# Optimization experiments

Measured on AMD Instinct MI355X. Metric: run time of the kernel, lower is better.

## Reference

```python
import jax, jax.numpy as jnp
from jax import lax
import numpy as np

B, N, C = 8, 50000, 8
SCORE_THR = 0.99
NMS_THR = 0.5
MAX_DET = 100
K_PRE = 1024          # per-class candidate budget (>> expected ~500 survivors of the 0.99 threshold)
NEG = jnp.float32(-1e30)


def setup_inputs() -> dict:
    key = jax.random.key(0)
    k1, k2, k3, k4, k5 = jax.random.split(key, 5)
    # valid (x1,y1,x2,y2) boxes in a 512px frame
    cxy = jax.random.uniform(k1, (B, N, 2), dtype=jnp.float32) * 512.0
    wh = jax.random.uniform(k2, (B, N, 2), dtype=jnp.float32) * 96.0 + 4.0
    boxes = jnp.concatenate([cxy - wh * 0.5, cxy + wh * 0.5], axis=-1)
    classification = jax.random.uniform(k3, (B, N, C), dtype=jnp.float32)
    rotation = jax.random.normal(k4, (B, N, 3), dtype=jnp.float32)
    translation = jax.random.normal(k5, (B, N, 3), dtype=jnp.float32)
    return {"boxes": boxes, "classification": classification,
            "rotation": rotation, "translation": translation}


def _pairwise_iou(b):  # b: [K,4] -> [K,K]
    x1, y1, x2, y2 = b[:, 0], b[:, 1], b[:, 2], b[:, 3]
    area = (x2 - x1) * (y2 - y1)
    iw = jnp.maximum(jnp.minimum(x2[:, None], x2[None, :]) - jnp.maximum(x1[:, None], x1[None, :]), 0.0)
    ih = jnp.maximum(jnp.minimum(y2[:, None], y2[None, :]) - jnp.maximum(y1[:, None], y1[None, :]), 0.0)
    inter = iw * ih
    return inter / (area[:, None] + area[None, :] - inter)


def _nms_one_class(boxes_n, scores_n):
    """boxes_n [N,4], scores_n [N] -> (top_s [K], top_i [K], keep [K] bool)."""
    masked = jnp.where(scores_n > SCORE_THR, scores_n, NEG)
    top_s, top_i = lax.top_k(masked, K_PRE)       # sorted descending, like torchvision NMS ordering
    cand = boxes_n[top_i]                          # [K,4]
    valid = top_s > SCORE_THR
    iou = _pairwise_iou(cand)                      # [K,K]

    def step(keep, i):
        # suppressed if any already-kept higher-score box overlaps > NMS_THR
        suppressed = jnp.any(keep & (iou[:, i] > NMS_THR))
        keep = keep.at[i].set(valid[i] & ~suppressed)
        return keep, None

    keep, _ = lax.scan(step, jnp.zeros(K_PRE, dtype=bool), jnp.arange(K_PRE))
    return top_s, top_i, keep


def _filter(boxes, classification, rotation, translation):
    b, n, c = classification.shape
    per_class = jax.vmap(_nms_one_class, in_axes=(None, 1))      # over classes
    top_s, top_i, keep = jax.vmap(per_class)(boxes, classification)  # [B,C,K] each

    sc = jnp.where(keep, top_s, NEG).reshape(b, c * K_PRE)
    labels = jnp.broadcast_to(jnp.arange(c)[None, :, None], (b, c, K_PRE)).reshape(b, c * K_PRE)
    idx = top_i.reshape(b, c * K_PRE)

    best_s, sel = lax.top_k(sc, MAX_DET)                          # [B,100]
    sel_idx = jnp.take_along_axis(idx, sel, axis=1)
    sel_lab = jnp.take_along_axis(labels, sel, axis=1)
    ok = best_s > SCORE_THR                                       # kept scores are all > threshold

    gather = lambda x: jnp.take_along_axis(x, sel_idx[:, :, None], axis=1)
    out_boxes = jnp.where(ok[:, :, None], gather(boxes), -1.0)
    out_scores = jnp.where(ok, best_s, -1.0)
    out_labels = jnp.where(ok, sel_lab, -1).astype(jnp.int64)
    out_rot = jnp.where(ok[:, :, None], gather(rotation), -1.0)
    out_trans = jnp.where(ok[:, :, None], gather(translation), -1.0)
    return out_boxes, out_scores, out_labels, out_rot, out_trans


@jax.jit
def reference(boxes, classification, rotation, translation):
    return _filter(boxes, classification, rotation, translation)
```

## Files before the change

### kernel.cpp

```cpp
#include <hip/hip_runtime.h>
#include <stdint.h>

#define BB 8
#define NN 50000
#define SCORE_THR 0.99f
#define NMS_THR 0.5f
#define MAX_DET 100
#define K_PRE 1024
#define CAP 2048
#define KEEP_CAP 128
#define CNT_STRIDE 64
#define T_MAX 16
#define NPAIR 136
#define TRI_WORDS 8704

typedef unsigned long long u64;
typedef unsigned int u32;
typedef __attribute__((ext_vector_type(2))) unsigned long long u64x2;


__global__ void k_init(int* __restrict__ cnts) {
    for (int i = threadIdx.x; i < 64 * CNT_STRIDE; i += 256) cnts[i] = 0;
}

__global__ __launch_bounds__(256) void k_filter(const float* __restrict__ cls,
                                                int* __restrict__ cand_cnt,
                                                u64* __restrict__ cand_keys) {
    __shared__ int wcnt[8][4];
    __shared__ int woff[8][4];
    __shared__ int cbase[8];
    int b = blockIdx.y;
    int tid = threadIdx.x;
    int lane = tid & 63, w = tid >> 6;
    int n = blockIdx.x * 256 + tid;
    bool vn = n < NN;
    float s[8];
    if (vn) {
        const float4* p = (const float4*)(cls + ((size_t)b * NN + n) * 8);
        float4 a = p[0], b2 = p[1];
        s[0] = a.x; s[1] = a.y; s[2] = a.z; s[3] = a.w;
        s[4] = b2.x; s[5] = b2.y; s[6] = b2.z; s[7] = b2.w;
    } else {
        #pragma unroll
        for (int c = 0; c < 8; ++c) s[c] = 0.f;
    }
    u64 bal[8];
    #pragma unroll
    for (int c = 0; c < 8; ++c) {
        bool pred = vn && (s[c] > SCORE_THR);
        bal[c] = __ballot(pred);
        if (lane == 0) wcnt[c][w] = (int)__popcll(bal[c]);
    }
    __syncthreads();
    if (tid < 8) {
        int c = tid, acc = 0;
        #pragma unroll
        for (int ww = 0; ww < 4; ++ww) { woff[c][ww] = acc; acc += wcnt[c][ww]; }
        cbase[c] = acc ? atomicAdd(&cand_cnt[(b * 8 + c) * CNT_STRIDE], acc) : 0;
    }
    __syncthreads();
    #pragma unroll
    for (int c = 0; c < 8; ++c) {
        if (vn && (s[c] > SCORE_THR)) {
            int slot = cbase[c] + woff[c][w] + (int)__popcll(bal[c] & ((1ull << lane) - 1ull));
            if (slot < CAP)
                cand_keys[(size_t)(b * 8 + c) * CAP + slot] =
                    ((u64)__float_as_uint(s[c]) << 32) | (u32)(~(u32)n);
        }
    }
}

__global__ __launch_bounds__(64) void k_sort(const float* __restrict__ boxes,
                                             const int* __restrict__ cand_cnt,
                                             const u64* __restrict__ cand_keys,
                                             u64* __restrict__ sk_g,
                                             float4* __restrict__ box4) {
    __shared__ __align__(16) u64 sk_in[CAP];
    int lane = threadIdx.x;
    int q = blockIdx.x;
    int bc = blockIdx.y;
    int b = bc >> 3;
    int cnt = cand_cnt[bc * CNT_STRIDE];
    if (cnt > CAP) cnt = CAP;
    if (q * 64 >= cnt) return;
    int cnt2 = (cnt + 1) & ~1;
    for (int i = lane; i < cnt2; i += 64)
        sk_in[i] = (i < cnt) ? cand_keys[(size_t)bc * CAP + i] : 0ull;
    __syncthreads();
    int i0 = q * 64 + lane;
    u64 k0 = (i0 < cnt) ? sk_in[i0] : 0ull;
    int r0 = 0;
    int nv = cnt2 >> 1;
    const u64x2* skv = (const u64x2*)sk_in;
    #pragma unroll 4
    for (int jv = 0; jv < nv; ++jv) {
        u64x2 kk = skv[jv];
        r0 += (kk.x > k0); r0 += (kk.y > k0);
    }
    if (i0 < cnt && r0 < K_PRE) {
        sk_g[(size_t)bc * K_PRE + r0] = k0;
        u32 n = ~(u32)k0;
        box4[(size_t)bc * K_PRE + r0] =
            *(const float4*)(boxes + ((size_t)b * NN + n) * 4);
    }
}

__global__ __launch_bounds__(256) void k_iou(const int* __restrict__ cand_cnt,
                                             const float4* __restrict__ box4,
                                             u64* __restrict__ rowmask) {
    int bc = blockIdx.y;
    int p = blockIdx.x;
    int cnt = cand_cnt[bc * CNT_STRIDE];
    int n_cand = cnt < K_PRE ? cnt : K_PRE;
    int ntiles = (n_cand + 63) >> 6;
    int ti = 0, acc = 0;
    while (acc + ti + 1 <= p) { acc += ti + 1; ++ti; }
    int tj = p - acc;
    if (ti >= ntiles) return;
    const float4* bx = box4 + (size_t)bc * K_PRE;
    __shared__ float4 srb[64];
    int tid = threadIdx.x;
    int lane = tid & 63, w = tid >> 6;
    if (tid < 64) srb[tid] = bx[ti * 64 + tid];
    __syncthreads();
    int cg = tj * 64 + lane;
    float4 cb = bx[cg];
    float ca = (cb.z - cb.x) * (cb.w - cb.y);
    u64* out = rowmask + (size_t)bc * TRI_WORDS + 64 * (ti * (ti + 1) / 2) + tj;
    #pragma unroll
    for (int r16 = 0; r16 < 16; ++r16) {
        int r = (w << 4) | r16;
        float4 rb = srb[r];
        float ra = (rb.z - rb.x) * (rb.w - rb.y);
        float iw = fminf(rb.z, cb.z) - fmaxf(rb.x, cb.x);
        float ih = fminf(rb.w, cb.w) - fmaxf(rb.y, cb.y);
        iw = fmaxf(iw, 0.f); ih = fmaxf(ih, 0.f);
        float inter = iw * ih;
        float iou = inter / (ra + ca - inter);
        int rg = ti * 64 + r;
        bool pr = (rg < n_cand) && (cg < n_cand) && ((ti != tj) || (lane < r)) &&
                  (iou > NMS_THR);
        u64 m = __ballot(pr);
        if (lane == 0) out[(size_t)r * (ti + 1)] = m;
    }
}

__global__ __launch_bounds__(1024) void k_fuse(const float* __restrict__ boxes,
                                               const float* __restrict__ rot,
                                               const float* __restrict__ trans,
                                               const int* __restrict__ cand_cnt,
                                               const u64* __restrict__ sk_g,
                                               const u64* __restrict__ rowmask,
                                               float* __restrict__ out) {
    __shared__ u64 fk[1024];
    __shared__ int scnt[8];
    int tid = threadIdx.x;
    int lane = tid & 63, w = tid >> 6;
    int b = blockIdx.x;
    fk[tid] = 0ull;
    __syncthreads();
    if (w < 8) {
        int c = w;
        int bc = b * 8 + c;
        int cnt = cand_cnt[bc * CNT_STRIDE];
        int n_cand = cnt < K_PRE ? cnt : K_PRE;
        int ntiles = (n_cand + 63) >> 6;
        const u64* tri = rowmask + (size_t)bc * TRI_WORDS;
        u64 kept_w[T_MAX];
        #pragma unroll
        for (int t = 0; t < T_MAX; ++t) kept_w[t] = 0ull;
        for (int t = 0; t < ntiles; ++t) {
            int g = t * 64 + lane;
            const u64* base = tri + 64 * (t * (t + 1) / 2) + (size_t)lane * (t + 1);
            u64 supbits = 0;
            #pragma unroll
            for (int ww = 0; ww < T_MAX - 1; ++ww)
                if (ww < t) supbits |= base[ww] & kept_w[ww];
            u64 rowm = base[t];
            bool el = (g < n_cand) && (supbits == 0ull);
            u64 alive = __ballot(el);
            u64 kb = 0;
            while (alive) {
                int j = __ffsll(alive) - 1;
                kb |= (1ull << j);
                u64 colj = __ballot(((rowm >> j) & 1ull) != 0);
                alive &= ~(colj | (1ull << j));
            }
            #pragma unroll
            for (int ww = 0; ww < T_MAX; ++ww)
                if (ww == t) kept_w[ww] = kb;
        }
        u64 lmask = (1ull << lane) - 1ull;
        int pre = 0;
        #pragma unroll
        for (int t = 0; t < T_MAX; ++t) {
            if (t < ntiles) {
                u64 kb = kept_w[t];
                if ((kb >> lane) & 1ull) {
                    int rank = pre + (int)__popcll(kb & lmask);
                    if (rank < KEEP_CAP) {
                        int i = t * 64 + lane;
                        u64 key = sk_g[(size_t)bc * K_PRE + i];
                        u32 sb = (u32)(key >> 32);
                        u32 n = (~(u32)key) & 0x1FFFFu;
                        int pos = c * K_PRE + i;
                        fk[c * KEEP_CAP + rank] =
                            ((u64)sb << 30) | ((u64)(8191 - pos) << 17) | (u64)n;
                    }
                }
                pre += (int)__popcll(kb);
            }
        }
        if (lane == 0) scnt[c] = pre < KEEP_CAP ? pre : KEEP_CAP;
    }
    __syncthreads();
    int c = tid >> 7, i = tid & 127;
    int cc = scnt[c];
    u64 key = fk[tid];
    int total = 0;
    #pragma unroll
    for (int r = 0; r < 8; ++r) total += scnt[r];
    if (i < cc) {
        int rank = i;
        #pragma unroll
        for (int r = 0; r < 8; ++r) {
            if (r == c) continue;
            int basei = r << 7;
            int lo;
            if (fk[basei + 127] > key) lo = 128;
            else {
                lo = 0;
                #pragma unroll
                for (int s = 64; s > 0; s >>= 1)
                    if (fk[basei + lo + s - 1] > key) lo += s;
            }
            rank += lo;
        }
        if (rank < MAX_DET) {
            u32 n = (u32)(key & 0x1FFFFu);
            int pos = 8191 - (int)((key >> 17) & 0x1FFFu);
            int cls = pos >> 10;
            float osc = __uint_as_float((u32)(key >> 30));
            const float* bp = boxes + ((size_t)b * NN + n) * 4;
            const float* rp = rot + ((size_t)b * NN + n) * 3;
            const float* tp = trans + ((size_t)b * NN + n) * 3;
            int base = b * MAX_DET + rank;
            out[base * 4 + 0] = bp[0];
            out[base * 4 + 1] = bp[1];
            out[base * 4 + 2] = bp[2];
            out[base * 4 + 3] = bp[3];
            out[BB * MAX_DET * 4 + base] = osc;
            out[BB * MAX_DET * 5 + base] = (float)cls;
            float* ro = out + BB * MAX_DET * 6;
            ro[base * 3 + 0] = rp[0];
            ro[base * 3 + 1] = rp[1];
            ro[base * 3 + 2] = rp[2];
            float* to = out + BB * MAX_DET * 6 + BB * MAX_DET * 3;
            to[base * 3 + 0] = tp[0];
            to[base * 3 + 1] = tp[1];
            to[base * 3 + 2] = tp[2];
        }
    }
    if (tid < MAX_DET && tid >= total) {
        int base = b * MAX_DET + tid;
        out[base * 4 + 0] = -1.f;
        out[base * 4 + 1] = -1.f;
        out[base * 4 + 2] = -1.f;
        out[base * 4 + 3] = -1.f;
        out[BB * MAX_DET * 4 + base] = -1.f;
        out[BB * MAX_DET * 5 + base] = -1.f;
        float* ro = out + BB * MAX_DET * 6;
        ro[base * 3 + 0] = -1.f;
        ro[base * 3 + 1] = -1.f;
        ro[base * 3 + 2] = -1.f;
        float* to = out + BB * MAX_DET * 6 + BB * MAX_DET * 3;
        to[base * 3 + 0] = -1.f;
        to[base * 3 + 1] = -1.f;
        to[base * 3 + 2] = -1.f;
    }
}

extern "C" void kernel_launch(void* const* d_in, const int* in_sizes, int n_in,
                              void* d_out, int out_size, void* d_ws, size_t ws_size,
                              hipStream_t stream) {
    const float* boxes = (const float*)d_in[0];
    const float* cls   = (const float*)d_in[1];
    const float* rot   = (const float*)d_in[2];
    const float* trans = (const float*)d_in[3];
    char* ws = (char*)d_ws;
    int* cand_cnt  = (int*)ws;
    u64* cand_keys = (u64*)(ws + 16896);
    u64* sk_g      = (u64*)(ws + 1065472);
    float4* box4   = (float4*)(ws + 1589760);
    u64* rowmask   = (u64*)(ws + 2638336);
    float* out = (float*)d_out;

    hipLaunchKernelGGL(k_init, dim3(1), dim3(256), 0, stream, cand_cnt);
    hipLaunchKernelGGL(k_filter, dim3((NN + 255) / 256, BB), dim3(256), 0, stream,
                       cls, cand_cnt, cand_keys);
    hipLaunchKernelGGL(k_sort, dim3(CAP / 64, 64), dim3(64), 0, stream,
                       boxes, cand_cnt, cand_keys, sk_g, box4);
    hipLaunchKernelGGL(k_iou, dim3(NPAIR, 64), dim3(256), 0, stream,
                       cand_cnt, box4, rowmask);
    hipLaunchKernelGGL(k_fuse, dim3(BB), dim3(1024), 0, stream,
                       boxes, rot, trans, cand_cnt, sk_g, rowmask, out);
}
```

Baseline: 144.2 us.

## Replace atomic compaction and rank sort with per-block slots and bucket sort

New measurement: 131.8 us. 8.6% less time.

```diff
diff --git a/kernel.cpp b/kernel.cpp
--- a/kernel.cpp
+++ b/kernel.cpp
@@ -9,30 +9,27 @@
 #define K_PRE 1024
 #define CAP 2048
 #define KEEP_CAP 128
-#define CNT_STRIDE 64
+#define NBLK 196
+#define SLOT_MAX 32
 #define T_MAX 16
 #define NPAIR 136
 #define TRI_WORDS 8704
+#define HB 2048
 
 typedef unsigned long long u64;
 typedef unsigned int u32;
-typedef __attribute__((ext_vector_type(2))) unsigned long long u64x2;
-
-
-__global__ void k_init(int* __restrict__ cnts) {
-    for (int i = threadIdx.x; i < 64 * CNT_STRIDE; i += 256) cnts[i] = 0;
-}
+
 
 __global__ __launch_bounds__(256) void k_filter(const float* __restrict__ cls,
-                                                int* __restrict__ cand_cnt,
-                                                u64* __restrict__ cand_keys) {
+                                                int* __restrict__ blkcnt,
+                                                u64* __restrict__ cand_blk) {
     __shared__ int wcnt[8][4];
     __shared__ int woff[8][4];
-    __shared__ int cbase[8];
+    int gx = blockIdx.x;
     int b = blockIdx.y;
     int tid = threadIdx.x;
     int lane = tid & 63, w = tid >> 6;
-    int n = blockIdx.x * 256 + tid;
+    int n = gx * 256 + tid;
     bool vn = n < NN;
     float s[8];
     if (vn) {
@@ -56,61 +53,134 @@
         int c = tid, acc = 0;
         #pragma unroll
         for (int ww = 0; ww < 4; ++ww) { woff[c][ww] = acc; acc += wcnt[c][ww]; }
-        cbase[c] = acc ? atomicAdd(&cand_cnt[(b * 8 + c) * CNT_STRIDE], acc) : 0;
+        blkcnt[(b * 8 + c) * NBLK + gx] = acc < SLOT_MAX ? acc : SLOT_MAX;
     }
     __syncthreads();
     #pragma unroll
     for (int c = 0; c < 8; ++c) {
         if (vn && (s[c] > SCORE_THR)) {
-            int slot = cbase[c] + woff[c][w] + (int)__popcll(bal[c] & ((1ull << lane) - 1ull));
-            if (slot < CAP)
-                cand_keys[(size_t)(b * 8 + c) * CAP + slot] =
+            int slot = woff[c][w] + (int)__popcll(bal[c] & ((1ull << lane) - 1ull));
+            if (slot < SLOT_MAX)
+                cand_blk[((size_t)(b * 8 + c) * NBLK + gx) * SLOT_MAX + slot] =
                     ((u64)__float_as_uint(s[c]) << 32) | (u32)(~(u32)n);
         }
     }
 }
 
-__global__ __launch_bounds__(64) void k_sort(const float* __restrict__ boxes,
-                                             const int* __restrict__ cand_cnt,
-                                             const u64* __restrict__ cand_keys,
-                                             u64* __restrict__ sk_g,
-                                             float4* __restrict__ box4) {
-    __shared__ __align__(16) u64 sk_in[CAP];
-    int lane = threadIdx.x;
-    int q = blockIdx.x;
-    int bc = blockIdx.y;
+__device__ __forceinline__ int bucket_of(u64 key) {
+    int bk = (int)(key >> 40) - 0x3F7D70;
+    return bk < 0 ? 0 : (bk > HB - 1 ? HB - 1 : bk);
+}
+
+__global__ __launch_bounds__(256) void k_sortB(const float* __restrict__ boxes,
+                                               const int* __restrict__ blkcnt,
+                                               const u64* __restrict__ cand_blk,
+                                               int* __restrict__ cnt_g,
+                                               u64* __restrict__ sk_g,
+                                               float4* __restrict__ box4) {
+    __shared__ int scntb[NBLK];
+    __shared__ int pref[NBLK];
+    __shared__ int cntTotS;
+    __shared__ __align__(16) u64 skin[CAP];
+    __shared__ __align__(16) u64 tmp[CAP];
+    __shared__ int hist[HB];
+    __shared__ int pre[HB];
+    __shared__ int offs[HB];
+    __shared__ int wsumS[4];
+    int tid = threadIdx.x;
+    int lane = tid & 63, w = tid >> 6;
+    int bc = blockIdx.x;
     int b = bc >> 3;
-    int cnt = cand_cnt[bc * CNT_STRIDE];
-    if (cnt > CAP) cnt = CAP;
-    if (q * 64 >= cnt) return;
-    int cnt2 = (cnt + 1) & ~1;
-    for (int i = lane; i < cnt2; i += 64)
-        sk_in[i] = (i < cnt) ? cand_keys[(size_t)bc * CAP + i] : 0ull;
-    __syncthreads();
-    int i0 = q * 64 + lane;
-    u64 k0 = (i0 < cnt) ? sk_in[i0] : 0ull;
-    int r0 = 0;
-    int nv = cnt2 >> 1;
-    const u64x2* skv = (const u64x2*)sk_in;
-    #pragma unroll 4
-    for (int jv = 0; jv < nv; ++jv) {
-        u64x2 kk = skv[jv];
-        r0 += (kk.x > k0); r0 += (kk.y > k0);
-    }
-    if (i0 < cnt && r0 < K_PRE) {
-        sk_g[(size_t)bc * K_PRE + r0] = k0;
-        u32 n = ~(u32)k0;
-        box4[(size_t)bc * K_PRE + r0] =
+    if (tid < NBLK) scntb[tid] = blkcnt[bc * NBLK + tid];
+    #pragma unroll
+    for (int k = 0; k < HB / 256; ++k) hist[tid + 256 * k] = 0;
+    __syncthreads();
+    if (w == 0) {
+        int carry = 0;
+        #pragma unroll
+        for (int r = 0; r < 4; ++r) {
+            int idx = r * 64 + lane;
+            int v = (idx < NBLK) ? scntb[idx] : 0;
+            int x = v;
+            #pragma unroll
+            for (int d = 1; d < 64; d <<= 1) {
+                int t = __shfl_up(x, d);
+                if (lane >= d) x += t;
+            }
+            if (idx < NBLK) pref[idx] = carry + x - v;
+            carry += __shfl(x, 63);
+        }
+        if (lane == 0) cntTotS = carry;
+    }
+    __syncthreads();
+    int cnt = cntTotS; if (cnt > CAP) cnt = CAP;
+    if (tid < NBLK) {
+        int cb = scntb[tid], base = pref[tid];
+        const u64* src = cand_blk + ((size_t)bc * NBLK + tid) * SLOT_MAX;
+        for (int k = 0; k < cb; ++k) {
+            int dst = base + k;
+            if (dst < CAP) skin[dst] = src[k];
+        }
+    }
+    __syncthreads();
+    for (int i = tid; i < cnt; i += 256) atomicAdd(&hist[bucket_of(skin[i])], 1);
+    __syncthreads();
+    int base8 = tid * (HB / 256);
+    int loc[HB / 256];
+    int s = 0;
+    #pragma unroll
+    for (int k = 0; k < HB / 256; ++k) { loc[k] = s; s += hist[base8 + k]; }
+    int x = s;
+    #pragma unroll
+    for (int d = 1; d < 64; d <<= 1) {
+        int t = __shfl_up(x, d);
+        if (lane >= d) x += t;
+    }
+    if (lane == 63) wsumS[w] = x;
+    __syncthreads();
+    int wbase = 0;
+    #pragma unroll
+    for (int ww = 0; ww < 4; ++ww) if (ww < w) wbase += wsumS[ww];
+    int tbase = wbase + x - s;
+    #pragma unroll
+    for (int k = 0; k < HB / 256; ++k) {
+        pre[base8 + k] = tbase + loc[k];
+        offs[base8 + k] = tbase + loc[k];
+    }
+    __syncthreads();
+    for (int i = tid; i < cnt; i += 256) {
+        u64 key = skin[i];
+        int pos = atomicAdd(&offs[bucket_of(key)], 1);
+        tmp[pos] = key;
+    }
+    __syncthreads();
+    for (int i = tid; i < cnt; i += 256) {
+        u64 key = tmp[i];
+        int bk = bucket_of(key);
+        int s0 = pre[bk], len = hist[bk];
+        int r = 0;
+        for (int j = s0; j < s0 + len; ++j) r += (tmp[j] > key);
+        int dst = (cnt - s0 - len) + r;
+        skin[dst] = key;
+    }
+    __syncthreads();
+    if (tid == 0) cnt_g[bc] = cnt;
+    int n_cand = cnt < K_PRE ? cnt : K_PRE;
+    for (int rr = tid; rr < n_cand; rr += 256) {
+        u64 key = skin[rr];
+        sk_g[(size_t)bc * K_PRE + rr] = key;
+        u32 n = ~(u32)key;
+        box4[(size_t)bc * K_PRE + rr] =
             *(const float4*)(boxes + ((size_t)b * NN + n) * 4);
     }
 }
 
-__global__ __launch_bounds__(256) void k_iou(const int* __restrict__ cand_cnt,
+__global__ __launch_bounds__(256) void k_iou(const int* __restrict__ cnt_g,
                                              const float4* __restrict__ box4,
                                              u64* __restrict__ rowmask) {
     int bc = blockIdx.y;
     int p = blockIdx.x;
-    int cnt = cand_cnt[bc * CNT_STRIDE];
+    int cnt = cnt_g[bc];
     int n_cand = cnt < K_PRE ? cnt : K_PRE;
     int ntiles = (n_cand + 63) >> 6;
     int ti = 0, acc = 0;
@@ -148,7 +218,7 @@
 __global__ __launch_bounds__(1024) void k_fuse(const float* __restrict__ boxes,
                                                const float* __restrict__ rot,
                                                const float* __restrict__ trans,
-                                               const int* __restrict__ cand_cnt,
+                                               const int* __restrict__ cnt_g,
                                                const u64* __restrict__ sk_g,
                                                const u64* __restrict__ rowmask,
                                                float* __restrict__ out) {
@@ -162,7 +232,7 @@
     if (w < 8) {
         int c = w;
         int bc = b * 8 + c;
-        int cnt = cand_cnt[bc * CNT_STRIDE];
+        int cnt = cnt_g[bc];
         int n_cand = cnt < K_PRE ? cnt : K_PRE;
         int ntiles = (n_cand + 63) >> 6;
         const u64* tri = rowmask + (size_t)bc * TRI_WORDS;
@@ -170,13 +240,13 @@
         #pragma unroll
         for (int t = 0; t < T_MAX; ++t) kept_w[t] = 0ull;
         for (int t = 0; t < ntiles; ++t) {
-            int g = t * 64 + lane;
             const u64* base = tri + 64 * (t * (t + 1) / 2) + (size_t)lane * (t + 1);
             u64 supbits = 0;
             #pragma unroll
             for (int ww = 0; ww < T_MAX - 1; ++ww)
                 if (ww < t) supbits |= base[ww] & kept_w[ww];
             u64 rowm = base[t];
+            int g = t * 64 + lane;
             bool el = (g < n_cand) && (supbits == 0ull);
             u64 alive = __ballot(el);
             u64 kb = 0;
@@ -288,20 +358,20 @@
     const float* rot   = (const float*)d_in[2];
     const float* trans = (const float*)d_in[3];
     char* ws = (char*)d_ws;
-    int* cand_cnt  = (int*)ws;
-    u64* cand_keys = (u64*)(ws + 16896);
-    u64* sk_g      = (u64*)(ws + 1065472);
-    float4* box4   = (float4*)(ws + 1589760);
-    u64* rowmask   = (u64*)(ws + 2638336);
+    int* blkcnt    = (int*)ws;
+    u64* cand_blk  = (u64*)(ws + 51200);
+    int* cnt_g     = (int*)(ws + 3262464);
+    u64* sk_g      = (u64*)(ws + 3262720);
+    float4* box4   = (float4*)(ws + 3787008);
+    u64* rowmask   = (u64*)(ws + 4835584);
     float* out = (float*)d_out;
 
-    hipLaunchKernelGGL(k_init, dim3(1), dim3(256), 0, stream, cand_cnt);
-    hipLaunchKernelGGL(k_filter, dim3((NN + 255) / 256, BB), dim3(256), 0, stream,
-                       cls, cand_cnt, cand_keys);
-    hipLaunchKernelGGL(k_sort, dim3(CAP / 64, 64), dim3(64), 0, stream,
-                       boxes, cand_cnt, cand_keys, sk_g, box4);
+    hipLaunchKernelGGL(k_filter, dim3(NBLK, BB), dim3(256), 0, stream,
+                       cls, blkcnt, cand_blk);
+    hipLaunchKernelGGL(k_sortB, dim3(64), dim3(256), 0, stream,
+                       boxes, blkcnt, cand_blk, cnt_g, sk_g, box4);
     hipLaunchKernelGGL(k_iou, dim3(NPAIR, 64), dim3(256), 0, stream,
-                       cand_cnt, box4, rowmask);
+                       cnt_g, box4, rowmask);
     hipLaunchKernelGGL(k_fuse, dim3(BB), dim3(1024), 0, stream,
-                       boxes, rot, trans, cand_cnt, sk_g, rowmask, out);
-}
+                       boxes, rot, trans, cnt_g, sk_g, rowmask, out);
+}
```
